# Kernel optimization log

Hardware: AMD Instinct MI355X
Metric: run time of the kernel (lower is better)

## Reference

```python
import jax, jax.numpy as jnp
import numpy as np

M, N = 64, 8192
IN_DIM, HID, OUT = 6, 256, 128


def _mlp3(x, params):
    # three Linear+ReLU layers
    for W, b in params:
        x = jax.nn.relu(x @ W + b)
    return x


def setup_inputs() -> dict:
    key = jax.random.key(0)
    ks = jax.random.split(key, 16)
    def lin(k, fan_in, fan_out):
        bound = 1.0 / np.sqrt(fan_in)
        kw, kb = jax.random.split(k)
        W = jax.random.uniform(kw, (fan_in, fan_out), jnp.float32, -bound, bound)
        b = jax.random.uniform(kb, (fan_out,), jnp.float32, -bound, bound)
        return W, b
    feat = jax.random.normal(ks[0], (M, N, IN_DIM), jnp.float32)
    eW1, eb1 = lin(ks[1], IN_DIM, HID)
    eW2, eb2 = lin(ks[2], HID, HID)
    eW3, eb3 = lin(ks[3], HID, HID)
    sW1, sb1 = lin(ks[4], HID, OUT)
    sW2, sb2 = lin(ks[5], OUT, OUT)
    sW3, sb3 = lin(ks[6], OUT, OUT)
    cW, cb = lin(ks[7], IN_DIM + HID + OUT, 1)
    return {
        'feat': feat,
        'eW1': eW1, 'eb1': eb1, 'eW2': eW2, 'eb2': eb2, 'eW3': eW3, 'eb3': eb3,
        'sW1': sW1, 'sb1': sb1, 'sW2': sW2, 'sb2': sb2, 'sW3': sW3, 'sb3': sb3,
        'cW': cW, 'cb': cb,
    }


def reference(feat, eW1, eb1, eW2, eb2, eW3, eb3,
              sW1, sb1, sW2, sb2, sW3, sb3, cW, cb):
    # embed MLP over all points: [M, N, HID]
    hidden = _mlp3(feat, [(eW1, eb1), (eW2, eb2), (eW3, eb3)])
    # max-pool over points within each bbox: [M, HID]
    pooled = jnp.max(hidden, axis=1)
    # segment MLP on pooled feature: [M, OUT]
    seg = _mlp3(pooled, [(sW1, sb1), (sW2, sb2), (sW3, sb3)])
    # concat [feat, hidden, seg broadcast over points]: [M, N, 6+HID+OUT]
    seg_tiled = jnp.broadcast_to(seg[:, None, :], (feat.shape[0], feat.shape[1], seg.shape[-1]))
    concat = jnp.concatenate([feat, hidden, seg_tiled], axis=-1)
    # classifier -> score [M, N]
    score = (concat @ cW)[..., 0] + cb[0]
    # per-bbox min/max rescale to [-1, 1]
    smin = jnp.min(score, axis=1, keepdims=True)
    smax = jnp.max(score, axis=1, keepdims=True)
    score = (score - smin) / (smax - smin) * 2.0 - 1.0
    return score
```

## Files before the change

kernel.cpp:

```cpp
#include <hip/hip_runtime.h>


typedef __attribute__((ext_vector_type(8))) short short8;
typedef __attribute__((ext_vector_type(4))) float f32x4;
typedef __attribute__((ext_vector_type(4))) unsigned int u32x4;

#define THREADS 512

__device__ __forceinline__ unsigned short f2bf(float f) {
  union { float f; unsigned int u; } x; x.f = f;
  unsigned int r = x.u + 0x7fffu + ((x.u >> 16) & 1u);
  return (unsigned short)(r >> 16);
}

__device__ __forceinline__ unsigned int cvt_pk_bf16(float lo, float hi) {
  unsigned int r;
  asm("v_cvt_pk_bf16_f32 %0, %1, %2" : "=v"(r) : "v"(lo), "v"(hi));
  return r;
}

__global__ void pn_pack(const float* __restrict__ W1,
                        const float* __restrict__ W2,
                        const float* __restrict__ W3,
                        unsigned short* __restrict__ wp) {
  int e = blockIdx.x * 256 + threadIdx.x;
  const float* src; int Kreal, base, r;
  if (e < 8192)       { src = W1; Kreal = 6;   base = 0;     r = e; }
  else if (e < 73728) { src = W2; Kreal = 256; base = 8192;  r = e - 8192; }
  else                { src = W3; Kreal = 256; base = 73728; r = e - 73728; }
  int j   = r & 7;
  int col = (r >> 3) & 15;
  int hi  = (r >> 7) & 3;
  int ct  = (r >> 9) & 15;
  int s   = r >> 13;
  int k = s * 32 + hi * 8 + j;
  int c = ct * 16 + col;
  float v = (k < Kreal) ? src[k * 256 + c] : 0.0f;
  wp[base + r] = f2bf(v);
}

__device__ __forceinline__ void gemm256(const unsigned short* __restrict__ wpL,
                                        const unsigned short* hbuf,
                                        int cgrp, int pgrp, int l15, int hi,
                                        f32x4 (&acc)[4][4]) {
#pragma unroll
  for (int ks = 0; ks < 8; ++ks) {
    short8 afr[4], bfr[4];
#pragma unroll
    for (int cf = 0; cf < 4; ++cf) {
      int ct = cgrp * 4 + cf;
      afr[cf] = *(const short8*)(wpL + (((((ks * 16 + ct) * 4) + hi) * 16 + l15) << 3));
    }
#pragma unroll
    for (int pf = 0; pf < 4; ++pf) {
      int p = pgrp * 64 + pf * 16 + l15;
      int byteoff = ((p * 256 + ks * 32 + hi * 8) * 2) ^ ((p & 7) << 4);
      bfr[pf] = *(const short8*)((const char*)hbuf + byteoff);
    }
#pragma unroll
    for (int cf = 0; cf < 4; ++cf)
#pragma unroll
      for (int pf = 0; pf < 4; ++pf)
        acc[cf][pf] = __builtin_amdgcn_mfma_f32_16x16x32_bf16(
            afr[cf], bfr[pf], acc[cf][pf], 0, 0, 0);
  }
}

__device__ __forceinline__ void epi_h(f32x4 (&acc)[4][4], unsigned short* dst,
                                      const float* bv,
                                      int cgrp, int pgrp, int l15, int hi) {
#pragma unroll
  for (int cf = 0; cf < 4; ++cf) {
    int c0 = cgrp * 64 + cf * 16 + hi * 4;
    float b0 = bv[c0], b1 = bv[c0 + 1], b2 = bv[c0 + 2], b3 = bv[c0 + 3];
#pragma unroll
    for (int pf = 0; pf < 4; ++pf) {
      int p = pgrp * 64 + pf * 16 + l15;
      f32x4 a = acc[cf][pf];
      unsigned int lo  = cvt_pk_bf16(fmaxf(a[0] + b0, 0.0f), fmaxf(a[1] + b1, 0.0f));
      unsigned int hi2 = cvt_pk_bf16(fmaxf(a[2] + b2, 0.0f), fmaxf(a[3] + b3, 0.0f));
      unsigned long long w = (unsigned long long)lo | ((unsigned long long)hi2 << 32);
      int byteoff = ((p * 256 + c0) * 2) ^ ((p & 7) << 4);
      *(unsigned long long*)((char*)dst + byteoff) = w;
    }
  }
}

__global__ __launch_bounds__(THREADS, 1) void pn_main(
    const float* __restrict__ feat,
    const unsigned short* __restrict__ wp,
    const float* __restrict__ b1,
    const float* __restrict__ b2,
    const float* __restrict__ b3,
    const float* __restrict__ cW,
    float* __restrict__ out) {
  __shared__ unsigned short hA[128 * 256];
  __shared__ unsigned short hF[128 * 8];
  __shared__ float biasL[3 * 256];
  __shared__ float whL[256];
  float* sPart = (float*)hF;

  const int tid  = threadIdx.x;
  const int lane = tid & 63;
  const int wave = tid >> 6;
  const int l15  = lane & 15;
  const int hi   = lane >> 4;
  const int cgrp = wave & 3;
  const int pgrp = wave >> 2;

  const int blk = blockIdx.x;
  const int m   = blk >> 6;
  const int n0  = (blk & 63) << 7;
  const int g0  = m * 8192 + n0;

  if (tid < 256) {
    biasL[tid]       = b1[tid];
    biasL[256 + tid] = b2[tid];
    biasL[512 + tid] = b3[tid];
    whL[tid]         = cW[6 + tid];
  }

  float fdot = 0.0f;
  if (tid < 128) {
    const float* fp = feat + (g0 + tid) * 6;
    float f0 = fp[0], f1 = fp[1], f2 = fp[2], f3 = fp[3], f4 = fp[4], f5 = fp[5];
    fdot = f0 * cW[0] + f1 * cW[1] + f2 * cW[2] + f3 * cW[3] + f4 * cW[4] + f5 * cW[5];
    u32x4 v;
    v[0] = cvt_pk_bf16(f0, f1);
    v[1] = cvt_pk_bf16(f2, f3);
    v[2] = cvt_pk_bf16(f4, f5);
    v[3] = 0;
    *(u32x4*)(hF + tid * 8) = v;
  }
  __syncthreads();

  f32x4 acc[4][4];
  const f32x4 zz = {0.f, 0.f, 0.f, 0.f};
  const short8 zero8 = {0, 0, 0, 0, 0, 0, 0, 0};

#pragma unroll
  for (int a = 0; a < 4; ++a)
#pragma unroll
    for (int b = 0; b < 4; ++b) acc[a][b] = zz;
  {
    short8 afr[4], bfr[4];
#pragma unroll
    for (int cf = 0; cf < 4; ++cf) {
      int ct = cgrp * 4 + cf;
      afr[cf] = *(const short8*)(wp + (((ct * 4 + hi) * 16 + l15) << 3));
    }
#pragma unroll
    for (int pf = 0; pf < 4; ++pf) {
      int p = pgrp * 64 + pf * 16 + l15;
      bfr[pf] = (hi == 0) ? *(const short8*)(hF + p * 8) : zero8;
    }
#pragma unroll
    for (int cf = 0; cf < 4; ++cf)
#pragma unroll
      for (int pf = 0; pf < 4; ++pf)
        acc[cf][pf] = __builtin_amdgcn_mfma_f32_16x16x32_bf16(
            afr[cf], bfr[pf], acc[cf][pf], 0, 0, 0);
  }
  epi_h(acc, hA, biasL + 0, cgrp, pgrp, l15, hi);
  __syncthreads();

#pragma unroll
  for (int a = 0; a < 4; ++a)
#pragma unroll
    for (int b = 0; b < 4; ++b) acc[a][b] = zz;
  gemm256(wp + 8192, hA, cgrp, pgrp, l15, hi, acc);
  __syncthreads();
  epi_h(acc, hA, biasL + 256, cgrp, pgrp, l15, hi);
  __syncthreads();

#pragma unroll
  for (int a = 0; a < 4; ++a)
#pragma unroll
    for (int b = 0; b < 4; ++b) acc[a][b] = zz;
  gemm256(wp + 73728, hA, cgrp, pgrp, l15, hi, acc);

  float part[4] = {0.f, 0.f, 0.f, 0.f};
#pragma unroll
  for (int cf = 0; cf < 4; ++cf) {
    int c0 = cgrp * 64 + cf * 16 + hi * 4;
#pragma unroll
    for (int r = 0; r < 4; ++r) {
      int c = c0 + r;
      float bb = biasL[512 + c];
      float wv = whL[c];
#pragma unroll
      for (int pf = 0; pf < 4; ++pf)
        part[pf] += fmaxf(acc[cf][pf][r] + bb, 0.0f) * wv;
    }
  }
#pragma unroll
  for (int off = 16; off < 64; off <<= 1)
#pragma unroll
    for (int pf = 0; pf < 4; ++pf)
      part[pf] += __shfl_xor(part[pf], off);
  if (hi == 0) {
#pragma unroll
    for (int pf = 0; pf < 4; ++pf)
      sPart[cgrp * 128 + pgrp * 64 + pf * 16 + l15] = part[pf];
  }
  __syncthreads();

  if (tid < 128) {
    float s = sPart[tid] + sPart[128 + tid] + sPart[256 + tid] + sPart[384 + tid]
            + fdot;
    out[g0 + tid] = s;
  }
}

__global__ void pn_finalize(float* __restrict__ out) {
  __shared__ float smn[4], smx[4];
  int mrow = blockIdx.x;
  float* row = out + mrow * 8192;
  float v[32];
  float mn = 1e30f, mx = -1e30f;
#pragma unroll
  for (int i = 0; i < 32; ++i) {
    v[i] = row[threadIdx.x + i * 256];
    mn = fminf(mn, v[i]);
    mx = fmaxf(mx, v[i]);
  }
#pragma unroll
  for (int off = 1; off < 64; off <<= 1) {
    mn = fminf(mn, __shfl_xor(mn, off));
    mx = fmaxf(mx, __shfl_xor(mx, off));
  }
  int w = threadIdx.x >> 6;
  if ((threadIdx.x & 63) == 0) { smn[w] = mn; smx[w] = mx; }
  __syncthreads();
  mn = fminf(fminf(smn[0], smn[1]), fminf(smn[2], smn[3]));
  mx = fmaxf(fmaxf(smx[0], smx[1]), fmaxf(smx[2], smx[3]));
  float sc = 2.0f / (mx - mn);
#pragma unroll
  for (int i = 0; i < 32; ++i)
    row[threadIdx.x + i * 256] = (v[i] - mn) * sc - 1.0f;
}

extern "C" void kernel_launch(void* const* d_in, const int* in_sizes, int n_in,
                              void* d_out, int out_size, void* d_ws, size_t ws_size,
                              hipStream_t stream) {
  const float* feat = (const float*)d_in[0];
  const float* eW1  = (const float*)d_in[1];
  const float* eb1  = (const float*)d_in[2];
  const float* eW2  = (const float*)d_in[3];
  const float* eb2  = (const float*)d_in[4];
  const float* eW3  = (const float*)d_in[5];
  const float* eb3  = (const float*)d_in[6];
  const float* cW   = (const float*)d_in[13];
  float* out = (float*)d_out;
  unsigned short* wpack = (unsigned short*)d_ws;

  pn_pack<<<544, 256, 0, stream>>>(eW1, eW2, eW3, wpack);
  pn_main<<<4096, THREADS, 0, stream>>>(feat, wpack, eb1, eb2, eb3, cW, out);
  pn_finalize<<<64, 256, 0, stream>>>(out);
}
```

Baseline: 145.1 us.

## Halve tile to 64 points per block and fold bias into accumulator init

Each block now handles 64 points with 4 waves instead of 128 points with 8 waves, which halves LDS use and doubles the grid. This lets several blocks reside per CU so barriers and epilogues can overlap with other blocks' MFMA work. Biases are now preloaded into the accumulators rather than added in the epilogue. The trade-off is that each weight fragment is reused across fewer points, so global/L2 weight traffic per point doubles.

```diff
diff --git a/kernel.cpp b/kernel.cpp
--- a/kernel.cpp
+++ b/kernel.cpp
@@ -5,7 +5,7 @@
 typedef __attribute__((ext_vector_type(4))) float f32x4;
 typedef __attribute__((ext_vector_type(4))) unsigned int u32x4;
 
-#define THREADS 512
+#define THREADS 256
 
 __device__ __forceinline__ unsigned short f2bf(float f) {
   union { float f; unsigned int u; } x; x.f = f;
@@ -41,7 +41,7 @@
 
 __device__ __forceinline__ void gemm256(const unsigned short* __restrict__ wpL,
                                         const unsigned short* hbuf,
-                                        int cgrp, int pgrp, int l15, int hi,
+                                        int cgrp, int l15, int hi,
                                         f32x4 (&acc)[4][4]) {
 #pragma unroll
   for (int ks = 0; ks < 8; ++ks) {
@@ -53,7 +53,7 @@
     }
 #pragma unroll
     for (int pf = 0; pf < 4; ++pf) {
-      int p = pgrp * 64 + pf * 16 + l15;
+      int p = pf * 16 + l15;
       int byteoff = ((p * 256 + ks * 32 + hi * 8) * 2) ^ ((p & 7) << 4);
       bfr[pf] = *(const short8*)((const char*)hbuf + byteoff);
     }
@@ -66,19 +66,27 @@
   }
 }
 
+__device__ __forceinline__ void acc_init(f32x4 (&acc)[4][4], const float* bv,
+                                         int cgrp, int hi) {
+#pragma unroll
+  for (int cf = 0; cf < 4; ++cf) {
+    f32x4 bi = *(const f32x4*)(bv + cgrp * 64 + cf * 16 + hi * 4);
+#pragma unroll
+    for (int pf = 0; pf < 4; ++pf) acc[cf][pf] = bi;
+  }
+}
+
 __device__ __forceinline__ void epi_h(f32x4 (&acc)[4][4], unsigned short* dst,
-                                      const float* bv,
-                                      int cgrp, int pgrp, int l15, int hi) {
+                                      int cgrp, int l15, int hi) {
 #pragma unroll
   for (int cf = 0; cf < 4; ++cf) {
     int c0 = cgrp * 64 + cf * 16 + hi * 4;
-    float b0 = bv[c0], b1 = bv[c0 + 1], b2 = bv[c0 + 2], b3 = bv[c0 + 3];
 #pragma unroll
     for (int pf = 0; pf < 4; ++pf) {
-      int p = pgrp * 64 + pf * 16 + l15;
+      int p = pf * 16 + l15;
       f32x4 a = acc[cf][pf];
-      unsigned int lo  = cvt_pk_bf16(fmaxf(a[0] + b0, 0.0f), fmaxf(a[1] + b1, 0.0f));
-      unsigned int hi2 = cvt_pk_bf16(fmaxf(a[2] + b2, 0.0f), fmaxf(a[3] + b3, 0.0f));
+      unsigned int lo  = cvt_pk_bf16(fmaxf(a[0], 0.0f), fmaxf(a[1], 0.0f));
+      unsigned int hi2 = cvt_pk_bf16(fmaxf(a[2], 0.0f), fmaxf(a[3], 0.0f));
       unsigned long long w = (unsigned long long)lo | ((unsigned long long)hi2 << 32);
       int byteoff = ((p * 256 + c0) * 2) ^ ((p & 7) << 4);
       *(unsigned long long*)((char*)dst + byteoff) = w;
@@ -94,8 +102,8 @@
     const float* __restrict__ b3,
     const float* __restrict__ cW,
     float* __restrict__ out) {
-  __shared__ unsigned short hA[128 * 256];
-  __shared__ unsigned short hF[128 * 8];
+  __shared__ unsigned short hA[64 * 256];
+  __shared__ unsigned short hF[64 * 8];
   __shared__ float biasL[3 * 256];
   __shared__ float whL[256];
   float* sPart = (float*)hF;
@@ -105,23 +113,20 @@
   const int wave = tid >> 6;
   const int l15  = lane & 15;
   const int hi   = lane >> 4;
-  const int cgrp = wave & 3;
-  const int pgrp = wave >> 2;
+  const int cgrp = wave;
 
   const int blk = blockIdx.x;
-  const int m   = blk >> 6;
-  const int n0  = (blk & 63) << 7;
+  const int m   = blk >> 7;
+  const int n0  = (blk & 127) << 6;
   const int g0  = m * 8192 + n0;
 
-  if (tid < 256) {
-    biasL[tid]       = b1[tid];
-    biasL[256 + tid] = b2[tid];
-    biasL[512 + tid] = b3[tid];
-    whL[tid]         = cW[6 + tid];
-  }
+  biasL[tid]       = b1[tid & 255];
+  biasL[256 + tid] = b2[tid & 255];
+  biasL[512 + tid] = b3[tid & 255];
+  whL[tid & 255]   = cW[6 + (tid & 255)];
 
   float fdot = 0.0f;
-  if (tid < 128) {
+  if (tid < 64) {
     const float* fp = feat + (g0 + tid) * 6;
     float f0 = fp[0], f1 = fp[1], f2 = fp[2], f3 = fp[3], f4 = fp[4], f5 = fp[5];
     fdot = f0 * cW[0] + f1 * cW[1] + f2 * cW[2] + f3 * cW[3] + f4 * cW[4] + f5 * cW[5];
@@ -135,13 +140,9 @@
   __syncthreads();
 
   f32x4 acc[4][4];
-  const f32x4 zz = {0.f, 0.f, 0.f, 0.f};
   const short8 zero8 = {0, 0, 0, 0, 0, 0, 0, 0};
 
-#pragma unroll
-  for (int a = 0; a < 4; ++a)
-#pragma unroll
-    for (int b = 0; b < 4; ++b) acc[a][b] = zz;
+  acc_init(acc, biasL + 0, cgrp, hi);
   {
     short8 afr[4], bfr[4];
 #pragma unroll
@@ -151,7 +152,7 @@
     }
 #pragma unroll
     for (int pf = 0; pf < 4; ++pf) {
-      int p = pgrp * 64 + pf * 16 + l15;
+      int p = pf * 16 + l15;
       bfr[pf] = (hi == 0) ? *(const short8*)(hF + p * 8) : zero8;
     }
 #pragma unroll
@@ -161,23 +162,17 @@
         acc[cf][pf] = __builtin_amdgcn_mfma_f32_16x16x32_bf16(
             afr[cf], bfr[pf], acc[cf][pf], 0, 0, 0);
   }
-  epi_h(acc, hA, biasL + 0, cgrp, pgrp, l15, hi);
-  __syncthreads();
-
-#pragma unroll
-  for (int a = 0; a < 4; ++a)
-#pragma unroll
-    for (int b = 0; b < 4; ++b) acc[a][b] = zz;
-  gemm256(wp + 8192, hA, cgrp, pgrp, l15, hi, acc);
-  __syncthreads();
-  epi_h(acc, hA, biasL + 256, cgrp, pgrp, l15, hi);
-  __syncthreads();
-
-#pragma unroll
-  for (int a = 0; a < 4; ++a)
-#pragma unroll
-    for (int b = 0; b < 4; ++b) acc[a][b] = zz;
-  gemm256(wp + 73728, hA, cgrp, pgrp, l15, hi, acc);
+  epi_h(acc, hA, cgrp, l15, hi);
+  __syncthreads();
+
+  acc_init(acc, biasL + 256, cgrp, hi);
+  gemm256(wp + 8192, hA, cgrp, l15, hi, acc);
+  __syncthreads();
+  epi_h(acc, hA, cgrp, l15, hi);
+  __syncthreads();
+
+  acc_init(acc, biasL + 512, cgrp, hi);
+  gemm256(wp + 73728, hA, cgrp, l15, hi, acc);
 
   float part[4] = {0.f, 0.f, 0.f, 0.f};
 #pragma unroll
@@ -185,12 +180,10 @@
     int c0 = cgrp * 64 + cf * 16 + hi * 4;
 #pragma unroll
     for (int r = 0; r < 4; ++r) {
-      int c = c0 + r;
-      float bb = biasL[512 + c];
-      float wv = whL[c];
+      float wv = whL[c0 + r];
 #pragma unroll
       for (int pf = 0; pf < 4; ++pf)
-        part[pf] += fmaxf(acc[cf][pf][r] + bb, 0.0f) * wv;
+        part[pf] += fmaxf(acc[cf][pf][r], 0.0f) * wv;
     }
   }
 #pragma unroll
@@ -201,12 +194,12 @@
   if (hi == 0) {
 #pragma unroll
     for (int pf = 0; pf < 4; ++pf)
-      sPart[cgrp * 128 + pgrp * 64 + pf * 16 + l15] = part[pf];
-  }
-  __syncthreads();
-
-  if (tid < 128) {
-    float s = sPart[tid] + sPart[128 + tid] + sPart[256 + tid] + sPart[384 + tid]
+      sPart[cgrp * 64 + pf * 16 + l15] = part[pf];
+  }
+  __syncthreads();
+
+  if (tid < 64) {
+    float s = sPart[tid] + sPart[64 + tid] + sPart[128 + tid] + sPart[192 + tid]
             + fdot;
     out[g0 + tid] = s;
   }
@@ -255,6 +248,6 @@
   unsigned short* wpack = (unsigned short*)d_ws;
 
   pn_pack<<<544, 256, 0, stream>>>(eW1, eW2, eW3, wpack);
-  pn_main<<<4096, THREADS, 0, stream>>>(feat, wpack, eb1, eb2, eb3, cW, out);
+  pn_main<<<8192, THREADS, 0, stream>>>(feat, wpack, eb1, eb2, eb3, cW, out);
   pn_finalize<<<64, 256, 0, stream>>>(out);
 }
```

After: 151.2 us. 1.04x slower.
